# Optimization experiments

Measured on AMD Instinct MI355X. Metric: run time of the kernel, lower is better.

Reference implementation:

```python
import jax, jax.numpy as jnp
import numpy as np

N, E = 100000, 1600000
DIMS = [128, 64, 64, 64, 32]  # in, hid, hid, hid, out
NEG_SLOPE = 0.2               # GATv2Conv default negative_slope
ELU_ALPHA_OUT = float(DIMS[-1])  # nn.ELU(out_channels): alpha = out_channels


def setup_inputs() -> dict:
    key = jax.random.key(0)
    ks = jax.random.split(key, 16)
    inp = {
        "x": jax.random.normal(ks[0], (N, DIMS[0]), dtype=jnp.float32),
        "edge_index": jax.random.randint(ks[1], (2, E), 0, N, dtype=jnp.int64),
    }
    ki = 2
    for i in range(4):
        fin, fout = DIMS[i], DIMS[i + 1]
        s = 1.0 / np.sqrt(fin)
        inp[f"Wl{i+1}"] = jax.random.uniform(ks[ki], (fin, fout), jnp.float32, -s, s); ki += 1
        inp[f"Wr{i+1}"] = jax.random.uniform(ks[ki], (fin, fout), jnp.float32, -s, s); ki += 1
        inp[f"att{i+1}"] = jax.random.uniform(ks[ki], (fout,), jnp.float32, -s, s); ki += 1
    return inp


def gatv2_layer(x, src, dst, Wl, Wr, att):
    # single head, concat=False, no self-loops, no bias (per module config)
    xl = x @ Wl                                   # [N, F] source-side projection
    xr = x @ Wr                                   # [N, F] target-side projection
    e = jax.nn.leaky_relu(xl[src] + xr[dst], NEG_SLOPE)   # [E, F]
    score = e @ att                               # [E]
    # softmax over incoming edges of each destination node
    m = jax.ops.segment_max(score, dst, num_segments=N)    # [N]
    ex = jnp.exp(score - m[dst])                  # [E]
    denom = jax.ops.segment_sum(ex, dst, num_segments=N)   # [N]
    alpha = ex / (denom[dst] + 1e-16)             # [E]
    # scatter-add weighted source messages
    return jax.ops.segment_sum(xl[src] * alpha[:, None], dst, num_segments=N)


def reference(x, edge_index, Wl1, Wr1, att1, Wl2, Wr2, att2, Wl3, Wr3, att3, Wl4, Wr4, att4):
    src, dst = edge_index[0], edge_index[1]
    h = jax.nn.elu(gatv2_layer(x, src, dst, Wl1, Wr1, att1))
    h = jax.nn.elu(gatv2_layer(h, src, dst, Wl2, Wr2, att2))
    h = jax.nn.elu(gatv2_layer(h, src, dst, Wl3, Wr3, att3))
    h = gatv2_layer(h, src, dst, Wl4, Wr4, att4)
    # nn.ELU(out_channels) -> ELU with alpha = out_channels (faithful quirk)
    return jnp.where(h > 0, h, ELU_ALPHA_OUT * jnp.expm1(h))
```

## Files before the change

kernel.cpp:

```cpp
#include <hip/hip_runtime.h>
#include <math.h>

typedef __attribute__((ext_vector_type(8))) short bf16x8;
typedef __attribute__((ext_vector_type(4))) float f32x4;
typedef __attribute__((ext_vector_type(2))) _Float16 h2;

#define BSHIFT 7
#define CH 8192

__device__ inline unsigned short f32_to_bf16_bits(float f) {
    unsigned int u = __float_as_uint(f);
    unsigned int r = (u + 0x7fffu + ((u >> 16) & 1u)) >> 16;
    return (unsigned short)r;
}
__device__ inline float bf16_bits_to_f32(unsigned short h) {
    return __uint_as_float(((unsigned int)h) << 16);
}
__device__ inline h2 u2h(unsigned u) { return __builtin_bit_cast(h2, u); }
__device__ inline unsigned h2u(h2 h) { return __builtin_bit_cast(unsigned, h); }

#define SWZ_ADD(t, imm) \
    t += __int_as_float(__builtin_amdgcn_ds_swizzle(__float_as_int(t), imm))

__device__ inline float dot2acc(h2 a, h2 b, float c) {
#if defined(__has_builtin)
#if __has_builtin(__builtin_amdgcn_fdot2)
    return __builtin_amdgcn_fdot2(a, b, c, false);
#else
    return c + (float)a[0] * (float)b[0] + (float)a[1] * (float)b[1];
#endif
#else
    return c + (float)a[0] * (float)b[0] + (float)a[1] * (float)b[1];
#endif
}


__global__ __launch_bounds__(256) void bucket_hist(
    const int* __restrict__ dst, int* __restrict__ bcnt8, int E, int nb, int nbp)
{
    __shared__ int h[1024];
    for (int i = threadIdx.x; i < nb; i += 256) h[i] = 0;
    __syncthreads();
    int e0 = blockIdx.x * CH, e1 = min(e0 + CH, E);
    for (int e = e0 + (int)threadIdx.x; e < e1; e += 256)
        atomicAdd(&h[dst[e] >> BSHIFT], 1);
    __syncthreads();
    int* mycnt = bcnt8 + (blockIdx.x & 7) * nbp;
    for (int b = threadIdx.x; b < nb; b += 256) {
        int c = h[b];
        if (c) atomicAdd(&mycnt[b], c);
    }
}

__global__ void bucket_scan(const int* __restrict__ bcnt8, int* __restrict__ bbase,
                            int* __restrict__ bcur8, int* __restrict__ rowstart,
                            int nb, int nbp, int E, int N)
{
    __shared__ int sh[1024];
    int t = threadIdx.x;
    int g8[8];
    int tot = 0;
#pragma unroll
    for (int g = 0; g < 8; ++g) {
        int c = (t < nb) ? bcnt8[g * nbp + t] : 0;
        g8[g] = c; tot += c;
    }
    sh[t] = tot;
    __syncthreads();
    for (int d = 1; d < 1024; d <<= 1) {
        int a = (t >= d) ? sh[t - d] : 0;
        __syncthreads();
        sh[t] += a;
        __syncthreads();
    }
    int base = sh[t] - tot;
    if (t <= nb) bbase[t] = base;
    if (t < nb) {
        int run = base;
#pragma unroll
        for (int g = 0; g < 8; ++g) { bcur8[g * nbp + t] = run; run += g8[g]; }
    }
    if (t == 0) rowstart[N] = E;
}

__global__ __launch_bounds__(256) void bucket_scatter(
    const int* __restrict__ src, const int* __restrict__ dst,
    int* __restrict__ bcur8, unsigned* __restrict__ pairs, int E, int nb, int nbp)
{
    __shared__ int h[1024];
    for (int i = threadIdx.x; i < nb; i += 256) h[i] = 0;
    __syncthreads();
    int e0 = blockIdx.x * CH, e1 = min(e0 + CH, E);
    for (int e = e0 + (int)threadIdx.x; e < e1; e += 256)
        atomicAdd(&h[dst[e] >> BSHIFT], 1);
    __syncthreads();
    int* mycur = bcur8 + (blockIdx.x & 7) * nbp;
    for (int b = threadIdx.x; b < nb; b += 256) {
        int c = h[b];
        if (c) h[b] = atomicAdd(&mycur[b], c);
    }
    __syncthreads();
    for (int e = e0 + (int)threadIdx.x; e < e1; e += 256) {
        int d = dst[e];
        int pos = atomicAdd(&h[d >> BSHIFT], 1);
        pairs[pos] = ((unsigned)src[e] << BSHIFT) | (unsigned)(d & 127);
    }
}

__global__ __launch_bounds__(256) void bucket_finalize(
    const unsigned* __restrict__ pairs, const int* __restrict__ bbase,
    int* __restrict__ rowstart, int* __restrict__ csr_src, int N)
{
    __shared__ int h[128];
    __shared__ int sh[256];
    int b = blockIdx.x;
    int p0 = bbase[b], p1 = bbase[b + 1];
    int t = threadIdx.x;
    if (t < 128) h[t] = 0;
    __syncthreads();
    for (int e = p0 + t; e < p1; e += 256)
        atomicAdd(&h[pairs[e] & 127], 1);
    __syncthreads();
    int v = (t < 128) ? h[t] : 0;
    sh[t] = v;
    __syncthreads();
    for (int d = 1; d < 256; d <<= 1) {
        int a = (t >= d) ? sh[t - d] : 0;
        __syncthreads();
        sh[t] += a;
        __syncthreads();
    }
    if (t < 128) {
        int off = sh[t] - v;
        int node = (b << BSHIFT) + t;
        if (node < N) rowstart[node] = p0 + off;
        h[t] = p0 + off;
    }
    __syncthreads();
    for (int e = p0 + t; e < p1; e += 256) {
        unsigned pr = pairs[e];
        int pos = atomicAdd(&h[pr & 127], 1);
        csr_src[pos] = (int)(pr >> BSHIFT);
    }
}


__global__ void prepack_kernel(const float* __restrict__ Wl, const float* __restrict__ Wr,
                               unsigned short* __restrict__ pWl, unsigned short* __restrict__ pWr,
                               int FIN, int FOUT) {
    int NT = FOUT >> 4, NK = FIN >> 5;
    int part = NT * NK * 512;
    int i = blockIdx.x * blockDim.x + threadIdx.x;
    int m = i / part;
    if (m >= 2) return;
    int ii = i - m * part;
    int j = ii & 7;
    int lane = (ii >> 3) & 63;
    int rest = ii >> 9;
    int ks = rest % NK;
    int t = rest / NK;
    int k = ks * 32 + (lane >> 4) * 8 + j;
    int c = t * 16 + (lane & 15);
    const float* W = m ? Wr : Wl;
    unsigned short* P = m ? pWr : pWl;
    float w = W[(size_t)k * FOUT + c];
    unsigned short hi = f32_to_bf16_bits(w);
    unsigned short lo = f32_to_bf16_bits(w - bf16_bits_to_f32(hi));
    P[ii] = hi;
    P[part + ii] = lo;
}


template<int FIN, int FOUT, bool IN16>
__global__ __launch_bounds__(256) void proj_mfma_kernel(
    const void* __restrict__ xin,
    const unsigned short* __restrict__ pWl, const unsigned short* __restrict__ pWr,
    const float* __restrict__ att,
    _Float16* __restrict__ xlh, _Float16* __restrict__ xrh,
    float* __restrict__ dl, float* __restrict__ dr, int n)
{
    constexpr int NT = FOUT >> 4;
    constexpr int NK = FIN >> 5;
    constexpr int PART = NT * NK * 512;
    const int wave = threadIdx.x >> 6;
    const int lane = threadIdx.x & 63;
    const int row0 = blockIdx.x * 64 + wave * 16;
    int arow = row0 + (lane & 15);
    if (arow >= n) arow = n - 1;
    const int khalf = lane >> 4;

    f32x4 accl[NT], accr[NT];
#pragma unroll
    for (int t = 0; t < NT; ++t) {
        accl[t] = (f32x4){0.f, 0.f, 0.f, 0.f};
        accr[t] = (f32x4){0.f, 0.f, 0.f, 0.f};
    }

#pragma unroll
    for (int ks = 0; ks < NK; ++ks) {
        float av[8];
        if (IN16) {
            const _Float16* xrow = (const _Float16*)xin + (size_t)arow * FIN + khalf * 8;
            float4 raw = *(const float4*)(xrow + ks * 32);
            const unsigned* u = (const unsigned*)&raw;
#pragma unroll
            for (int j = 0; j < 4; ++j) {
                h2 p = u2h(u[j]);
                av[2 * j]     = (float)p[0];
                av[2 * j + 1] = (float)p[1];
            }
        } else {
            const float* xrow = (const float*)xin + (size_t)arow * FIN + khalf * 8;
            float4 a0 = *(const float4*)(xrow + ks * 32);
            float4 a1 = *(const float4*)(xrow + ks * 32 + 4);
            av[0] = a0.x; av[1] = a0.y; av[2] = a0.z; av[3] = a0.w;
            av[4] = a1.x; av[5] = a1.y; av[6] = a1.z; av[7] = a1.w;
        }
        bf16x8 ah, al;
#pragma unroll
        for (int j = 0; j < 8; ++j) {
            unsigned short h = f32_to_bf16_bits(av[j]);
            ah[j] = (short)h;
            al[j] = (short)f32_to_bf16_bits(av[j] - bf16_bits_to_f32(h));
        }
#pragma unroll
        for (int t = 0; t < NT; ++t) {
            const unsigned short* bpl = pWl + ((size_t)(t * NK + ks) * 64 + lane) * 8;
            bf16x8 bh  = *(const bf16x8*)bpl;
            bf16x8 blo = *(const bf16x8*)(bpl + PART);
            accl[t] = __builtin_amdgcn_mfma_f32_16x16x32_bf16(ah, bh,  accl[t], 0, 0, 0);
            accl[t] = __builtin_amdgcn_mfma_f32_16x16x32_bf16(ah, blo, accl[t], 0, 0, 0);
            accl[t] = __builtin_amdgcn_mfma_f32_16x16x32_bf16(al, bh,  accl[t], 0, 0, 0);
            const unsigned short* bpr = pWr + ((size_t)(t * NK + ks) * 64 + lane) * 8;
            bh  = *(const bf16x8*)bpr;
            blo = *(const bf16x8*)(bpr + PART);
            accr[t] = __builtin_amdgcn_mfma_f32_16x16x32_bf16(ah, bh,  accr[t], 0, 0, 0);
            accr[t] = __builtin_amdgcn_mfma_f32_16x16x32_bf16(ah, blo, accr[t], 0, 0, 0);
            accr[t] = __builtin_amdgcn_mfma_f32_16x16x32_bf16(al, bh,  accr[t], 0, 0, 0);
        }
    }

    const int orow0 = row0 + khalf * 4;
    const int colb = lane & 15;
    float attc[NT];
#pragma unroll
    for (int t = 0; t < NT; ++t) attc[t] = att[t * 16 + colb];

#pragma unroll
    for (int t = 0; t < NT; ++t) {
        int col = t * 16 + colb;
#pragma unroll
        for (int r = 0; r < 4; ++r) {
            int rr = orow0 + r;
            if (rr < n) {
                xlh[(size_t)rr * FOUT + col] = (_Float16)accl[t][r];
                xrh[(size_t)rr * FOUT + col] = (_Float16)accr[t][r];
            }
        }
    }
#pragma unroll
    for (int r = 0; r < 4; ++r) {
        float pl = 0.f, pr = 0.f;
#pragma unroll
        for (int t = 0; t < NT; ++t) { pl += accl[t][r] * attc[t]; pr += accr[t][r] * attc[t]; }
#pragma unroll
        for (int off = 1; off < 16; off <<= 1) {
            pl += __shfl_xor(pl, off);
            pr += __shfl_xor(pr, off);
        }
        int rr = orow0 + r;
        if (colb == 0 && rr < n) { dl[rr] = pl; dr[rr] = pr; }
    }
}


template<int F, int AMODE, bool OUT16>
__global__ __launch_bounds__(256) void agg_kernel(
    const _Float16* __restrict__ xlh, const _Float16* __restrict__ xrh,
    const float* __restrict__ att,
    const float* __restrict__ dl, const float* __restrict__ dr,
    const int* __restrict__ rowstart, const int* __restrict__ csr_src,
    void* __restrict__ outv, int n, int E, int ntiles)
{
    constexpr int LPE = F / 8;
    constexpr int LSH = (F == 64) ? 6 : 5;
    constexpr int NPG = 64 / LPE;

    int wv0  = (blockIdx.x * blockDim.x + threadIdx.x) >> 6;
    int nwaves = gridDim.x * (blockDim.x >> 6);
    int lane = threadIdx.x & 63;
    int grp = lane / LPE;
    int fl  = lane % LPE;

    h2 atth[4];
#pragma unroll
    for (int j = 0; j < 4; ++j) {
        atth[j][0] = (_Float16)att[fl * 8 + 2 * j];
        atth[j][1] = (_Float16)att[fl * 8 + 2 * j + 1];
    }

    for (int tile = wv0; tile < ntiles; tile += nwaves) {
        int node = tile * NPG + grp;
        bool act = node < n;
        int nc = act ? node : 0;

        float4 xrraw = *(const float4*)(xrh + (((unsigned)nc << LSH) + fl * 8));
        h2 xrv[4];
#pragma unroll
        for (int j = 0; j < 4; ++j) xrv[j] = u2h(((const unsigned*)&xrraw)[j]);
        float cdr = 0.6f * dr[nc];

        int s0 = rowstart[nc];
        int s1 = act ? rowstart[nc + 1] : s0;
        int s1c = min(max(s1 - 1, s0), E - 1);

        float m = -1e30f, mth = -1e30f, ssum = 0.f;
        float o[8];
#pragma unroll
        for (int j = 0; j < 8; ++j) o[j] = 0.f;

        int cA0 = csr_src[min(s0,     s1c)];
        int cB0 = csr_src[min(s0 + 1, s1c)];
        int cA1 = csr_src[min(s0 + 2, s1c)];
        int cB1 = csr_src[min(s0 + 3, s1c)];
        float4 rA0 = *(const float4*)(xlh + (((unsigned)cA0 << LSH) + fl * 8));
        float4 rB0 = *(const float4*)(xlh + (((unsigned)cB0 << LSH) + fl * 8));
        float  dA0 = dl[cA0], dB0 = dl[cB0];
        float4 rA1 = *(const float4*)(xlh + (((unsigned)cA1 << LSH) + fl * 8));
        float4 rB1 = *(const float4*)(xlh + (((unsigned)cB1 << LSH) + fl * 8));
        float  dA1 = dl[cA1], dB1 = dl[cB1];
        int fA0 = csr_src[min(s0 + 4, s1c)];
        int fB0 = csr_src[min(s0 + 5, s1c)];
        int fA1 = csr_src[min(s0 + 6, s1c)];
        int fB1 = csr_src[min(s0 + 7, s1c)];

        int i0 = s0;

#define AGG_COMPUTE(RA, RB, DA, DB)                                          \
        {                                                                    \
            h2 a[4], b[4];                                                   \
            _Pragma("unroll")                                                \
            for (int j = 0; j < 4; ++j) {                                    \
                a[j] = u2h(((const unsigned*)&RA)[j]);                       \
                b[j] = u2h(((const unsigned*)&RB)[j]);                       \
            }                                                                \
            bool vb = (i0 + 1) < s1;                                         \
            float ta = 0.f, tb = 0.f;                                        \
            _Pragma("unroll")                                                \
            for (int j = 0; j < 4; ++j) {                                    \
                h2 ea = a[j] + xrv[j];                                       \
                h2 eb = b[j] + xrv[j];                                       \
                ea = u2h(h2u(ea) & 0x7FFF7FFFu);                             \
                eb = u2h(h2u(eb) & 0x7FFF7FFFu);                             \
                ta = dot2acc(atth[j], ea, ta);                               \
                tb = dot2acc(atth[j], eb, tb);                               \
            }                                                                \
            SWZ_ADD(ta, 0x041F); SWZ_ADD(tb, 0x041F);                        \
            SWZ_ADD(ta, 0x081F); SWZ_ADD(tb, 0x081F);                        \
            if (LPE == 8) { SWZ_ADD(ta, 0x101F); SWZ_ADD(tb, 0x101F); }      \
            float pa = 0.6f * DA + cdr + 0.4f * ta;                          \
            float pb = vb ? (0.6f * DB + cdr + 0.4f * tb) : -1e30f;          \
            float pm = fmaxf(pa, pb);                                        \
            if (pm > mth) {                                                  \
                float c = __expf(m - pm);                                    \
                ssum *= c;                                                   \
                _Pragma("unroll")                                            \
                for (int j = 0; j < 8; ++j) o[j] *= c;                       \
                m = pm; mth = pm + 8.0f;                                     \
            }                                                                \
            float wa = __expf(pa - m);                                       \
            float wb = __expf(pb - m);                                       \
            ssum += wa + wb;                                                 \
            _Pragma("unroll")                                                \
            for (int j = 0; j < 4; ++j) {                                    \
                o[2 * j]     += wa * (float)a[j][0] + wb * (float)b[j][0];   \
                o[2 * j + 1] += wa * (float)a[j][1] + wb * (float)b[j][1];   \
            }                                                                \
        }

        while (i0 < s1) {
            {
                int cA2 = fA0, cB2 = fB0;
                fA0 = csr_src[min(i0 + 8, s1c)];
                fB0 = csr_src[min(i0 + 9, s1c)];
                AGG_COMPUTE(rA0, rB0, dA0, dB0);
                rA0 = *(const float4*)(xlh + (((unsigned)cA2 << LSH) + fl * 8));
                rB0 = *(const float4*)(xlh + (((unsigned)cB2 << LSH) + fl * 8));
                dA0 = dl[cA2]; dB0 = dl[cB2];
            }
            i0 += 2;
            if (i0 >= s1) break;
            {
                int cA2 = fA1, cB2 = fB1;
                fA1 = csr_src[min(i0 + 8, s1c)];
                fB1 = csr_src[min(i0 + 9, s1c)];
                AGG_COMPUTE(rA1, rB1, dA1, dB1);
                rA1 = *(const float4*)(xlh + (((unsigned)cA2 << LSH) + fl * 8));
                rB1 = *(const float4*)(xlh + (((unsigned)cB2 << LSH) + fl * 8));
                dA1 = dl[cA2]; dB1 = dl[cB2];
            }
            i0 += 2;
        }
#undef AGG_COMPUTE

        float inv = 1.f / (ssum + 1e-16f);
        float res[8];
#pragma unroll
        for (int j = 0; j < 8; ++j) {
            float r = o[j] * inv;
            if (AMODE == 1) r = (r > 0.f) ? r : expm1f(r);
            else            r = (r > 0.f) ? r : 32.f * expm1f(r);
            res[j] = r;
        }
        if (act) {
            if (OUT16) {
                unsigned pk[4];
#pragma unroll
                for (int j = 0; j < 4; ++j) {
                    h2 t;
                    t[0] = (_Float16)res[2 * j];
                    t[1] = (_Float16)res[2 * j + 1];
                    pk[j] = h2u(t);
                }
                _Float16* op = (_Float16*)outv + (((unsigned)node << LSH) + fl * 8);
                *(float4*)op = *(const float4*)pk;
            } else {
                float* op = (float*)outv + (((unsigned)node << LSH) + fl * 8);
                *(float4*)op       = (float4){res[0], res[1], res[2], res[3]};
                *(float4*)(op + 4) = (float4){res[4], res[5], res[6], res[7]};
            }
        }
    }
}


extern "C" void kernel_launch(void* const* d_in, const int* in_sizes, int n_in,
                              void* d_out, int out_size, void* d_ws, size_t ws_size,
                              hipStream_t stream) {
    const float* x    = (const float*)d_in[0];
    const int*   ei   = (const int*)d_in[1];
    const float* Wl1  = (const float*)d_in[2];
    const float* Wr1  = (const float*)d_in[3];
    const float* att1 = (const float*)d_in[4];
    const float* Wl2  = (const float*)d_in[5];
    const float* Wr2  = (const float*)d_in[6];
    const float* att2 = (const float*)d_in[7];
    const float* Wl3  = (const float*)d_in[8];
    const float* Wr3  = (const float*)d_in[9];
    const float* att3 = (const float*)d_in[10];
    const float* Wl4  = (const float*)d_in[11];
    const float* Wr4  = (const float*)d_in[12];
    const float* att4 = (const float*)d_in[13];

    const int N = in_sizes[0] / 128;
    const int E = in_sizes[1] / 2;
    const int* src = ei;
    const int* dst = ei + E;

    const int nb  = (N + 127) >> BSHIFT;
    const int nbp = (nb + 15) & ~15;

    char* w = (char*)d_ws;
    size_t off = 0;
    auto take = [&](size_t bytes) -> void* {
        void* p = w + off;
        off = (off + bytes + 255) & ~(size_t)255;
        return p;
    };
    int* bcnt8    = (int*)take((size_t)8 * nbp * 4);
    int* bcur8    = (int*)take((size_t)8 * nbp * 4);
    int* bbase    = (int*)take((size_t)(nb + 1) * 4);
    int* rowstart = (int*)take((size_t)(N + 1) * 4);
    int* csr_src  = (int*)take((size_t)E * 4);
    float* dl = (float*)take((size_t)N * 4);
    float* dr = (float*)take((size_t)N * 4);
    _Float16* xlh = (_Float16*)take((size_t)N * 64 * 2);
    _Float16* xrh = (_Float16*)take((size_t)N * 64 * 2);
    _Float16* hA  = (_Float16*)take((size_t)N * 64 * 2);
    _Float16* hB  = (_Float16*)take((size_t)N * 64 * 2);
    unsigned short* pWl1 = (unsigned short*)take(2 * 4 * 4 * 512 * 2);
    unsigned short* pWr1 = (unsigned short*)take(2 * 4 * 4 * 512 * 2);
    unsigned short* pWl2 = (unsigned short*)take(2 * 4 * 2 * 512 * 2);
    unsigned short* pWr2 = (unsigned short*)take(2 * 4 * 2 * 512 * 2);
    unsigned short* pWl3 = (unsigned short*)take(2 * 4 * 2 * 512 * 2);
    unsigned short* pWr3 = (unsigned short*)take(2 * 4 * 2 * 512 * 2);
    unsigned short* pWl4 = (unsigned short*)take(2 * 2 * 2 * 512 * 2);
    unsigned short* pWr4 = (unsigned short*)take(2 * 2 * 2 * 512 * 2);
    unsigned* pairs = (unsigned*)hA;
    float* outf = (float*)d_out;

    hipMemsetAsync(bcnt8, 0, (size_t)8 * nbp * 4, stream);

    prepack_kernel<<<(2 * 4 * 4 * 512 + 255) / 256, 256, 0, stream>>>(Wl1, Wr1, pWl1, pWr1, 128, 64);
    prepack_kernel<<<(2 * 4 * 2 * 512 + 255) / 256, 256, 0, stream>>>(Wl2, Wr2, pWl2, pWr2, 64, 64);
    prepack_kernel<<<(2 * 4 * 2 * 512 + 255) / 256, 256, 0, stream>>>(Wl3, Wr3, pWl3, pWr3, 64, 64);
    prepack_kernel<<<(2 * 2 * 2 * 512 + 255) / 256, 256, 0, stream>>>(Wl4, Wr4, pWl4, pWr4, 64, 32);

    int kgrid = (E + CH - 1) / CH;
    bucket_hist<<<kgrid, 256, 0, stream>>>(dst, bcnt8, E, nb, nbp);
    bucket_scan<<<1, 1024, 0, stream>>>(bcnt8, bbase, bcur8, rowstart, nb, nbp, E, N);
    bucket_scatter<<<kgrid, 256, 0, stream>>>(src, dst, bcur8, pairs, E, nb, nbp);
    bucket_finalize<<<nb, 256, 0, stream>>>(pairs, bbase, rowstart, csr_src, N);

    int pblk = (N + 63) / 64;
    const int AGGB = 2048;
    int nt64 = (N + 7) / 8;
    int nt32 = (N + 15) / 16;

    proj_mfma_kernel<128, 64, false><<<pblk, 256, 0, stream>>>(x, pWl1, pWr1, att1, xlh, xrh, dl, dr, N);
    agg_kernel<64, 1, true><<<AGGB, 256, 0, stream>>>(xlh, xrh, att1, dl, dr, rowstart, csr_src, hA, N, E, nt64);

    proj_mfma_kernel<64, 64, true><<<pblk, 256, 0, stream>>>(hA, pWl2, pWr2, att2, xlh, xrh, dl, dr, N);
    agg_kernel<64, 1, true><<<AGGB, 256, 0, stream>>>(xlh, xrh, att2, dl, dr, rowstart, csr_src, hB, N, E, nt64);

    proj_mfma_kernel<64, 64, true><<<pblk, 256, 0, stream>>>(hB, pWl3, pWr3, att3, xlh, xrh, dl, dr, N);
    agg_kernel<64, 1, true><<<AGGB, 256, 0, stream>>>(xlh, xrh, att3, dl, dr, rowstart, csr_src, hA, N, E, nt64);

    proj_mfma_kernel<64, 32, true><<<pblk, 256, 0, stream>>>(hA, pWl4, pWr4, att4, xlh, xrh, dl, dr, N);
    agg_kernel<32, 2, false><<<AGGB, 256, 0, stream>>>(xlh, xrh, att4, dl, dr, rowstart, csr_src, outf, N, E, nt32);
}
```

Baseline: 295.8 us.

## Sort CSR neighbor lists, merge prepack launches, use atomic tile scheduling in aggregation

Three separate changes. Each destination's source list in the CSR is now insertion-sorted so neighbor gathers run in ascending address order, aiming for better cache locality. The four weight-prepack launches become one kernel, saving launch overhead. The aggregation kernels fetch tiles through a global atomic counter instead of a static grid-stride loop, to balance uneven degrees across waves. The serial per-node insertion sort, about 16 edges per node, adds work to the CSR build, and the atomic counter adds contention.

```diff
diff --git a/kernel.cpp b/kernel.cpp
--- a/kernel.cpp
+++ b/kernel.cpp
@@ -130,11 +130,13 @@
         sh[t] += a;
         __syncthreads();
     }
+    int segstart = 0;
     if (t < 128) {
         int off = sh[t] - v;
         int node = (b << BSHIFT) + t;
-        if (node < N) rowstart[node] = p0 + off;
-        h[t] = p0 + off;
+        segstart = p0 + off;
+        if (node < N) rowstart[node] = segstart;
+        h[t] = segstart;
     }
     __syncthreads();
     for (int e = p0 + t; e < p1; e += 256) {
@@ -142,18 +144,26 @@
         int pos = atomicAdd(&h[pr & 127], 1);
         csr_src[pos] = (int)(pr >> BSHIFT);
     }
-}
-
-
-__global__ void prepack_kernel(const float* __restrict__ Wl, const float* __restrict__ Wr,
-                               unsigned short* __restrict__ pWl, unsigned short* __restrict__ pWr,
-                               int FIN, int FOUT) {
+    __syncthreads();
+    if (t < 128) {
+        int segend = h[t];
+        for (int i = segstart + 1; i < segend; ++i) {
+            int val = csr_src[i];
+            int j = i - 1;
+            while (j >= segstart && csr_src[j] > val) {
+                csr_src[j + 1] = csr_src[j];
+                --j;
+            }
+            csr_src[j + 1] = val;
+        }
+    }
+}
+
+
+__device__ inline void prepack_one(const float* __restrict__ W, unsigned short* __restrict__ P,
+                                   int FIN, int FOUT, int ii) {
     int NT = FOUT >> 4, NK = FIN >> 5;
     int part = NT * NK * 512;
-    int i = blockIdx.x * blockDim.x + threadIdx.x;
-    int m = i / part;
-    if (m >= 2) return;
-    int ii = i - m * part;
     int j = ii & 7;
     int lane = (ii >> 3) & 63;
     int rest = ii >> 9;
@@ -161,13 +171,28 @@
     int t = rest / NK;
     int k = ks * 32 + (lane >> 4) * 8 + j;
     int c = t * 16 + (lane & 15);
-    const float* W = m ? Wr : Wl;
-    unsigned short* P = m ? pWr : pWl;
     float w = W[(size_t)k * FOUT + c];
     unsigned short hi = f32_to_bf16_bits(w);
     unsigned short lo = f32_to_bf16_bits(w - bf16_bits_to_f32(hi));
     P[ii] = hi;
     P[part + ii] = lo;
+}
+
+__global__ void prepack_all(
+    const float* Wl1, const float* Wr1, const float* Wl2, const float* Wr2,
+    const float* Wl3, const float* Wr3, const float* Wl4, const float* Wr4,
+    unsigned short* pWl1, unsigned short* pWr1, unsigned short* pWl2, unsigned short* pWr2,
+    unsigned short* pWl3, unsigned short* pWr3, unsigned short* pWl4, unsigned short* pWr4)
+{
+    int i = blockIdx.x * 256 + threadIdx.x;
+    if      (i < 8192)  prepack_one(Wl1, pWl1, 128, 64, i);
+    else if (i < 16384) prepack_one(Wr1, pWr1, 128, 64, i - 8192);
+    else if (i < 20480) prepack_one(Wl2, pWl2, 64, 64, i - 16384);
+    else if (i < 24576) prepack_one(Wr2, pWr2, 64, 64, i - 20480);
+    else if (i < 28672) prepack_one(Wl3, pWl3, 64, 64, i - 24576);
+    else if (i < 32768) prepack_one(Wr3, pWr3, 64, 64, i - 28672);
+    else if (i < 34816) prepack_one(Wl4, pWl4, 64, 32, i - 32768);
+    else if (i < 36864) prepack_one(Wr4, pWr4, 64, 32, i - 34816);
 }
 
 
@@ -280,14 +305,12 @@
     const float* __restrict__ att,
     const float* __restrict__ dl, const float* __restrict__ dr,
     const int* __restrict__ rowstart, const int* __restrict__ csr_src,
-    void* __restrict__ outv, int n, int E, int ntiles)
+    void* __restrict__ outv, int* __restrict__ ctr, int n, int E, int ntiles)
 {
     constexpr int LPE = F / 8;
     constexpr int LSH = (F == 64) ? 6 : 5;
     constexpr int NPG = 64 / LPE;
 
-    int wv0  = (blockIdx.x * blockDim.x + threadIdx.x) >> 6;
-    int nwaves = gridDim.x * (blockDim.x >> 6);
     int lane = threadIdx.x & 63;
     int grp = lane / LPE;
     int fl  = lane % LPE;
@@ -299,7 +322,12 @@
         atth[j][1] = (_Float16)att[fl * 8 + 2 * j + 1];
     }
 
-    for (int tile = wv0; tile < ntiles; tile += nwaves) {
+    for (;;) {
+        int tile = 0;
+        if (lane == 0) tile = atomicAdd(ctr, 1);
+        tile = __shfl(tile, 0);
+        if (tile >= ntiles) break;
+
         int node = tile * NPG + grp;
         bool act = node < n;
         int nc = act ? node : 0;
@@ -472,6 +500,7 @@
     int* bbase    = (int*)take((size_t)(nb + 1) * 4);
     int* rowstart = (int*)take((size_t)(N + 1) * 4);
     int* csr_src  = (int*)take((size_t)E * 4);
+    int* ctrs     = (int*)take(64);
     float* dl = (float*)take((size_t)N * 4);
     float* dr = (float*)take((size_t)N * 4);
     _Float16* xlh = (_Float16*)take((size_t)N * 64 * 2);
@@ -490,11 +519,10 @@
     float* outf = (float*)d_out;
 
     hipMemsetAsync(bcnt8, 0, (size_t)8 * nbp * 4, stream);
-
-    prepack_kernel<<<(2 * 4 * 4 * 512 + 255) / 256, 256, 0, stream>>>(Wl1, Wr1, pWl1, pWr1, 128, 64);
-    prepack_kernel<<<(2 * 4 * 2 * 512 + 255) / 256, 256, 0, stream>>>(Wl2, Wr2, pWl2, pWr2, 64, 64);
-    prepack_kernel<<<(2 * 4 * 2 * 512 + 255) / 256, 256, 0, stream>>>(Wl3, Wr3, pWl3, pWr3, 64, 64);
-    prepack_kernel<<<(2 * 2 * 2 * 512 + 255) / 256, 256, 0, stream>>>(Wl4, Wr4, pWl4, pWr4, 64, 32);
+    hipMemsetAsync(ctrs, 0, 64, stream);
+
+    prepack_all<<<144, 256, 0, stream>>>(Wl1, Wr1, Wl2, Wr2, Wl3, Wr3, Wl4, Wr4,
+                                         pWl1, pWr1, pWl2, pWr2, pWl3, pWr3, pWl4, pWr4);
 
     int kgrid = (E + CH - 1) / CH;
     bucket_hist<<<kgrid, 256, 0, stream>>>(dst, bcnt8, E, nb, nbp);
@@ -508,14 +536,14 @@
     int nt32 = (N + 15) / 16;
 
     proj_mfma_kernel<128, 64, false><<<pblk, 256, 0, stream>>>(x, pWl1, pWr1, att1, xlh, xrh, dl, dr, N);
-    agg_kernel<64, 1, true><<<AGGB, 256, 0, stream>>>(xlh, xrh, att1, dl, dr, rowstart, csr_src, hA, N, E, nt64);
+    agg_kernel<64, 1, true><<<AGGB, 256, 0, stream>>>(xlh, xrh, att1, dl, dr, rowstart, csr_src, hA, ctrs + 0, N, E, nt64);
 
     proj_mfma_kernel<64, 64, true><<<pblk, 256, 0, stream>>>(hA, pWl2, pWr2, att2, xlh, xrh, dl, dr, N);
-    agg_kernel<64, 1, true><<<AGGB, 256, 0, stream>>>(xlh, xrh, att2, dl, dr, rowstart, csr_src, hB, N, E, nt64);
+    agg_kernel<64, 1, true><<<AGGB, 256, 0, stream>>>(xlh, xrh, att2, dl, dr, rowstart, csr_src, hB, ctrs + 1, N, E, nt64);
 
     proj_mfma_kernel<64, 64, true><<<pblk, 256, 0, stream>>>(hB, pWl3, pWr3, att3, xlh, xrh, dl, dr, N);
-    agg_kernel<64, 1, true><<<AGGB, 256, 0, stream>>>(xlh, xrh, att3, dl, dr, rowstart, csr_src, hA, N, E, nt64);
+    agg_kernel<64, 1, true><<<AGGB, 256, 0, stream>>>(xlh, xrh, att3, dl, dr, rowstart, csr_src, hA, ctrs + 2, N, E, nt64);
 
     proj_mfma_kernel<64, 32, true><<<pblk, 256, 0, stream>>>(hA, pWl4, pWr4, att4, xlh, xrh, dl, dr, N);
-    agg_kernel<32, 2, false><<<AGGB, 256, 0, stream>>>(xlh, xrh, att4, dl, dr, rowstart, csr_src, outf, N, E, nt32);
-}
+    agg_kernel<32, 2, false><<<AGGB, 256, 0, stream>>>(xlh, xrh, att4, dl, dr, rowstart, csr_src, outf, ctrs + 3, N, E, nt32);
+}
```

Result: slower. 1.139 ms (+285.2%).
